# Kernel tuning notes

Measured on AMD Instinct MI355X. Metric: run time of the kernel, lower is better.

## Reference

```python
import jax, jax.numpy as jnp
import numpy as np
from jax import lax

HIDDEN = 10
LAYERS = 5
IN_SIZE = 2
OUT_SIZE = 1
BATCH = 4096
SEQ = 512


def _lstm_layer(xs, h0, c0, W_ih, W_hh, b):
    # xs: [T, B, in], h0/c0: [B, H], W_ih: [4H, in], W_hh: [4H, H], b: [4H]
    def step(carry, x_t):
        h, c = carry
        g = x_t @ W_ih.T + h @ W_hh.T + b  # [B, 4H]
        i, f, gg, o = jnp.split(g, 4, axis=-1)  # torch gate order: i, f, g, o
        i = jax.nn.sigmoid(i)
        f = jax.nn.sigmoid(f)
        gg = jnp.tanh(gg)
        o = jax.nn.sigmoid(o)
        c_new = f * c + i * gg
        h_new = o * jnp.tanh(c_new)
        return (h_new, c_new), h_new

    (hT, cT), hs = lax.scan(step, (h0, c0), xs)
    return hs, hT, cT


def setup_inputs() -> dict:
    key = jax.random.key(0)
    ks = jax.random.split(key, 8)
    s = 1.0 / np.sqrt(HIDDEN)  # torch LSTM init scale
    x = jax.random.normal(ks[0], (BATCH, SEQ, IN_SIZE), dtype=jnp.float32)
    h = jnp.zeros((LAYERS, BATCH, HIDDEN), dtype=jnp.float32)
    c = jnp.zeros((LAYERS, BATCH, HIDDEN), dtype=jnp.float32)
    W_ih0 = jax.random.uniform(ks[1], (4 * HIDDEN, IN_SIZE), minval=-s, maxval=s, dtype=jnp.float32)
    W_ih_rest = jax.random.uniform(ks[2], (LAYERS - 1, 4 * HIDDEN, HIDDEN), minval=-s, maxval=s, dtype=jnp.float32)
    W_hh = jax.random.uniform(ks[3], (LAYERS, 4 * HIDDEN, HIDDEN), minval=-s, maxval=s, dtype=jnp.float32)
    # combined b_ih + b_hh (mathematically identical to torch's two biases)
    b = jax.random.uniform(ks[4], (LAYERS, 4 * HIDDEN), minval=-2 * s, maxval=2 * s, dtype=jnp.float32)
    Wf = jax.random.uniform(ks[5], (OUT_SIZE, HIDDEN), minval=-s, maxval=s, dtype=jnp.float32)
    bf = jax.random.uniform(ks[6], (OUT_SIZE,), minval=-s, maxval=s, dtype=jnp.float32)
    return {"x": x, "h": h, "c": c, "W_ih0": W_ih0, "W_ih_rest": W_ih_rest,
            "W_hh": W_hh, "b": b, "Wf": Wf, "bf": bf}


def reference(x, h, c, W_ih0, W_ih_rest, W_hh, b, Wf, bf):
    xs = jnp.transpose(x, (1, 0, 2))  # [T, B, in] (batch_first -> time-major)
    h_outs, c_outs = [], []
    hs, hT, cT = _lstm_layer(xs, h[0], c[0], W_ih0, W_hh[0], b[0])
    h_outs.append(hT); c_outs.append(cT)
    for l in range(1, LAYERS):
        hs, hT, cT = _lstm_layer(hs, h[l], c[l], W_ih_rest[l - 1], W_hh[l], b[l])
        h_outs.append(hT); c_outs.append(cT)
    L1 = jnp.transpose(hs, (1, 0, 2))  # [B, T, H]
    out = jax.nn.sigmoid(L1 @ Wf.T + bf)  # [B, T, 1]
    return out, (jnp.stack(h_outs), jnp.stack(c_outs))
```

## Files before the change

### kernel.cpp

```cpp
#include <hip/hip_runtime.h>

#define B_ 4096
#define T_ 512
#define H_ 10
#define L_ 5
#define LOG2E 1.44269504f

#define SLOTF(g)   ((g) * 12)
#define TRASH_OFF  72
#define XBUF_OFF   88
#define XENT       520
#define LDS_FLOATS (XBUF_OFF + XENT * 4)

__device__ __forceinline__ float sigm2(float xs) {
    return __builtin_amdgcn_rcpf(1.0f + __builtin_amdgcn_exp2f(-xs));
}
__device__ __forceinline__ float tanh2(float xs) {
    return fmaf(-2.0f, __builtin_amdgcn_rcpf(__builtin_amdgcn_exp2f(xs) + 1.0f), 1.0f);
}

#define DOT10(acc, W, A, Bv, Cv)                              \
    acc = fmaf(W[0], A.x,  acc); acc = fmaf(W[1], A.y,  acc); \
    acc = fmaf(W[2], A.z,  acc); acc = fmaf(W[3], A.w,  acc); \
    acc = fmaf(W[4], Bv.x, acc); acc = fmaf(W[5], Bv.y, acc); \
    acc = fmaf(W[6], Bv.z, acc); acc = fmaf(W[7], Bv.w, acc); \
    acc = fmaf(W[8], Cv.x, acc); acc = fmaf(W[9], Cv.y, acc);

#define GATES(S, GUARD, OUTST)                                                 \
  {                                                                            \
    const float4 xA = *(const float4*)(prevp);                                 \
    const float4 xB = *(const float4*)(prevp + 4);                             \
    const float2 xC = *(const float2*)(prevp + 8);                             \
    const float4 hA = *(const float4*)(ownp);                                  \
    const float4 hB = *(const float4*)(ownp + 4);                              \
    const float2 hC = *(const float2*)(ownp + 8);                              \
    float a0 = bs4[0], a1 = bs4[1], a2 = bs4[2], a3 = bs4[3];                  \
    DOT10(a0, wih[0], xA, xB, xC)                                              \
    DOT10(a1, wih[1], xA, xB, xC)                                              \
    DOT10(a2, wih[2], xA, xB, xC)                                              \
    DOT10(a3, wih[3], xA, xB, xC)                                              \
    DOT10(a0, whh[0], hA, hB, hC)                                              \
    DOT10(a1, whh[1], hA, hB, hC)                                              \
    DOT10(a2, whh[2], hA, hB, hC)                                              \
    DOT10(a3, whh[3], hA, hB, hC)                                              \
    const float ig = sigm2(a0), fg = sigm2(a1);                                \
    const float gg = tanh2(a2), og = sigm2(a3);                                \
    const float cn = fmaf(fg, c, ig * gg);                                     \
    const float hn = og * tanh2(cn * (2.0f * LOG2E));                          \
    if (GUARD) {                                                               \
      const int tl = (S) - g;                                                  \
      const bool valid = (unsigned)tl < (unsigned)T_;                          \
      float* wrt = valid ? wrp : trashp;                                       \
      *wrt = hn;                                                               \
      if (valid) c = cn;                                                       \
      if ((g < 5) && (tl == T_ - 1)) {                                         \
        out[(size_t)(B_ * T_) + g * (B_ * H_) + b * H_ + j] = hn;              \
        out[(size_t)(B_ * T_) + (size_t)(L_ * B_ * H_)                         \
            + g * (B_ * H_) + b * H_ + j] = cn;                                \
      }                                                                        \
    } else {                                                                   \
      *wrp = hn;                                                               \
      c = cn;                                                                  \
    }                                                                          \
    if (OUTST) {                                                               \
      if (g == 5) out[(size_t)b * T_ + ((S) - 5)] = ig;                        \
    }                                                                          \
    prevp += pinc;                                                             \
  }

__global__ __launch_bounds__(64, 3)
void lstm5(const float* __restrict__ x,
           const float* __restrict__ h0,
           const float* __restrict__ c0,
           const float* __restrict__ Wih0,
           const float* __restrict__ WihR,
           const float* __restrict__ Whh,
           const float* __restrict__ bias,
           const float* __restrict__ Wf,
           const float* __restrict__ bfp,
           float* __restrict__ out)
{
    __shared__ __align__(16) float lds[LDS_FLOATS];

    const int lane = threadIdx.x;
    const int g = lane / 10;
    const int j = lane - g * 10;
    const int b = blockIdx.x;

    {
        const float2* x2 = (const float2*)(x + (size_t)b * (T_ * 2));
        #pragma unroll
        for (int i = 0; i < 8; ++i) {
            const int idx = i * 64 + lane;
            float2 v = x2[idx];
            *(float4*)&lds[XBUF_OFF + idx * 4] = make_float4(v.x, v.y, 0.0f, 0.0f);
        }
        if (lane < 8)  lds[XBUF_OFF + 512 * 4 + lane] = 0.0f;
        if (lane < 12) lds[SLOTF(5) + lane] = 0.0f;
    }

    const float scq[4] = {LOG2E, LOG2E, 2.0f * LOG2E, LOG2E};
    float wih[4][10], whh[4][10], bs4[4];
    #pragma unroll
    for (int q = 0; q < 4; ++q) {
        bs4[q] = 0.0f;
        #pragma unroll
        for (int k = 0; k < 10; ++k) { wih[q][k] = 0.0f; whh[q][k] = 0.0f; }
    }
    if (g < 5) {
        #pragma unroll
        for (int q = 0; q < 4; ++q) {
            const int row = q * H_ + j;
            const float sc = scq[q];
            bs4[q] = bias[g * 40 + row] * sc;
            #pragma unroll
            for (int k = 0; k < 10; ++k)
                whh[q][k] = Whh[g * 400 + row * 10 + k] * sc;
            if (g == 0) {
                wih[q][0] = Wih0[row * 2 + 0] * sc;
                wih[q][1] = Wih0[row * 2 + 1] * sc;
            } else {
                #pragma unroll
                for (int k = 0; k < 10; ++k)
                    wih[q][k] = WihR[(g - 1) * 400 + row * 10 + k] * sc;
            }
        }
    } else if (g == 5) {
        #pragma unroll
        for (int k = 0; k < 10; ++k) wih[0][k] = Wf[k] * LOG2E;
        bs4[0] = bfp[0] * LOG2E;
    }

    float c = 0.0f;
    if (g < 5) {
        c = c0[g * (B_ * H_) + b * H_ + j];
        lds[SLOTF(g) + j] = h0[g * (B_ * H_) + b * H_ + j];
    }
    __syncthreads();

    float* ownp  = &lds[(g < 5) ? SLOTF(g) : SLOTF(5)];
    float* prevp = (g == 0) ? &lds[XBUF_OFF]
                 : (g <= 5) ? &lds[SLOTF(g - 1)]
                            : &lds[SLOTF(5)];
    float* wrp   = (g < 5) ? &lds[SLOTF(g) + j]
                           : &lds[TRASH_OFF + (lane - 50)];
    float* trashp = &lds[TRASH_OFF + (lane & 15)];
    const int pinc = (g == 0) ? 4 : 0;

    for (int s = 0; s < 5; ++s)        GATES(s, true,  false)
    for (int s = 5; s <= 510; ++s)     GATES(s, false, true )
    for (int s = 511; s <= 516; ++s)   GATES(s, true,  true )
}

extern "C" void kernel_launch(void* const* d_in, const int* in_sizes, int n_in,
                              void* d_out, int out_size, void* d_ws, size_t ws_size,
                              hipStream_t stream) {
    const float* x    = (const float*)d_in[0];
    const float* h0   = (const float*)d_in[1];
    const float* c0   = (const float*)d_in[2];
    const float* Wih0 = (const float*)d_in[3];
    const float* WihR = (const float*)d_in[4];
    const float* Whh  = (const float*)d_in[5];
    const float* bias = (const float*)d_in[6];
    const float* Wf   = (const float*)d_in[7];
    const float* bf   = (const float*)d_in[8];
    float* out = (float*)d_out;

    dim3 grid(B_);
    dim3 block(64);
    hipLaunchKernelGGL(lstm5, grid, block, 0, stream,
                       x, h0, c0, Wih0, WihR, Whh, bias, Wf, bf, out);
}
```

Measured before the change: 375.1 us.

## Process two batch rows per wavefront using packed FP32 FMA instructions

```diff
diff --git a/kernel.cpp b/kernel.cpp
--- a/kernel.cpp
+++ b/kernel.cpp
@@ -1,4 +1,7 @@
 #include <hip/hip_runtime.h>
+
+typedef float v2f __attribute__((ext_vector_type(2)));
+typedef float v4f __attribute__((ext_vector_type(4)));
 
 #define B_ 4096
 #define T_ 512
@@ -6,69 +9,99 @@
 #define L_ 5
 #define LOG2E 1.44269504f
 
-#define SLOTF(g)   ((g) * 12)
-#define TRASH_OFF  72
-#define XBUF_OFF   88
-#define XENT       520
-#define LDS_FLOATS (XBUF_OFF + XENT * 4)
-
-__device__ __forceinline__ float sigm2(float xs) {
-    return __builtin_amdgcn_rcpf(1.0f + __builtin_amdgcn_exp2f(-xs));
-}
-__device__ __forceinline__ float tanh2(float xs) {
-    return fmaf(-2.0f, __builtin_amdgcn_rcpf(__builtin_amdgcn_exp2f(xs) + 1.0f), 1.0f);
-}
-
-#define DOT10(acc, W, A, Bv, Cv)                              \
-    acc = fmaf(W[0], A.x,  acc); acc = fmaf(W[1], A.y,  acc); \
-    acc = fmaf(W[2], A.z,  acc); acc = fmaf(W[3], A.w,  acc); \
-    acc = fmaf(W[4], Bv.x, acc); acc = fmaf(W[5], Bv.y, acc); \
-    acc = fmaf(W[6], Bv.z, acc); acc = fmaf(W[7], Bv.w, acc); \
-    acc = fmaf(W[8], Cv.x, acc); acc = fmaf(W[9], Cv.y, acc);
-
-#define GATES(S, GUARD, OUTST)                                                 \
-  {                                                                            \
-    const float4 xA = *(const float4*)(prevp);                                 \
-    const float4 xB = *(const float4*)(prevp + 4);                             \
-    const float2 xC = *(const float2*)(prevp + 8);                             \
-    const float4 hA = *(const float4*)(ownp);                                  \
-    const float4 hB = *(const float4*)(ownp + 4);                              \
-    const float2 hC = *(const float2*)(ownp + 8);                              \
-    float a0 = bs4[0], a1 = bs4[1], a2 = bs4[2], a3 = bs4[3];                  \
-    DOT10(a0, wih[0], xA, xB, xC)                                              \
-    DOT10(a1, wih[1], xA, xB, xC)                                              \
-    DOT10(a2, wih[2], xA, xB, xC)                                              \
-    DOT10(a3, wih[3], xA, xB, xC)                                              \
-    DOT10(a0, whh[0], hA, hB, hC)                                              \
-    DOT10(a1, whh[1], hA, hB, hC)                                              \
-    DOT10(a2, whh[2], hA, hB, hC)                                              \
-    DOT10(a3, whh[3], hA, hB, hC)                                              \
-    const float ig = sigm2(a0), fg = sigm2(a1);                                \
-    const float gg = tanh2(a2), og = sigm2(a3);                                \
-    const float cn = fmaf(fg, c, ig * gg);                                     \
-    const float hn = og * tanh2(cn * (2.0f * LOG2E));                          \
-    if (GUARD) {                                                               \
-      const int tl = (S) - g;                                                  \
-      const bool valid = (unsigned)tl < (unsigned)T_;                          \
-      float* wrt = valid ? wrp : trashp;                                       \
-      *wrt = hn;                                                               \
-      if (valid) c = cn;                                                       \
-      if ((g < 5) && (tl == T_ - 1)) {                                         \
-        out[(size_t)(B_ * T_) + g * (B_ * H_) + b * H_ + j] = hn;              \
-        out[(size_t)(B_ * T_) + (size_t)(L_ * B_ * H_)                         \
-            + g * (B_ * H_) + b * H_ + j] = cn;                                \
-      }                                                                        \
-    } else {                                                                   \
-      *wrp = hn;                                                               \
-      c = cn;                                                                  \
-    }                                                                          \
-    if (OUTST) {                                                               \
-      if (g == 5) out[(size_t)b * T_ + ((S) - 5)] = ig;                        \
-    }                                                                          \
-    prevp += pinc;                                                             \
+#define SLOTF(g)   ((g) * 28)
+#define TRASH_F    168
+#define XBUF_F     200
+#define LDS_FLOATS (XBUF_F + 520 * 4)
+
+__device__ __forceinline__ v2f pk_fma(v2f a, v2f b, v2f c) {
+    v2f d;
+    asm("v_pk_fma_f32 %0, %1, %2, %3" : "=v"(d) : "v"(a), "v"(b), "v"(c));
+    return d;
+}
+__device__ __forceinline__ v2f pk_mul(v2f a, v2f b) {
+    v2f d;
+    asm("v_pk_mul_f32 %0, %1, %2" : "=v"(d) : "v"(a), "v"(b));
+    return d;
+}
+__device__ __forceinline__ v2f pk_add(v2f a, v2f b) {
+    v2f d;
+    asm("v_pk_add_f32 %0, %1, %2" : "=v"(d) : "v"(a), "v"(b));
+    return d;
+}
+
+__device__ __forceinline__ v2f sigm2p(v2f xs) {
+    v2f r;
+    r.x = __builtin_amdgcn_rcpf(1.0f + __builtin_amdgcn_exp2f(-xs.x));
+    r.y = __builtin_amdgcn_rcpf(1.0f + __builtin_amdgcn_exp2f(-xs.y));
+    return r;
+}
+__device__ __forceinline__ v2f tanh2p(v2f xs) {
+    v2f r;
+    r.x = fmaf(-2.0f, __builtin_amdgcn_rcpf(__builtin_amdgcn_exp2f(xs.x) + 1.0f), 1.0f);
+    r.y = fmaf(-2.0f, __builtin_amdgcn_rcpf(__builtin_amdgcn_exp2f(xs.y) + 1.0f), 1.0f);
+    return r;
+}
+
+#define DOTX(acc, W)                                                  \
+    acc = pk_fma(W[0], q0.lo, acc); acc = pk_fma(W[1], q0.hi, acc);   \
+    acc = pk_fma(W[2], q1.lo, acc); acc = pk_fma(W[3], q1.hi, acc);   \
+    acc = pk_fma(W[4], q2.lo, acc); acc = pk_fma(W[5], q2.hi, acc);   \
+    acc = pk_fma(W[6], q3.lo, acc); acc = pk_fma(W[7], q3.hi, acc);   \
+    acc = pk_fma(W[8], q4.lo, acc); acc = pk_fma(W[9], q4.hi, acc);
+#define DOTH(acc, W)                                                  \
+    acc = pk_fma(W[0], r0.lo, acc); acc = pk_fma(W[1], r0.hi, acc);   \
+    acc = pk_fma(W[2], r1.lo, acc); acc = pk_fma(W[3], r1.hi, acc);   \
+    acc = pk_fma(W[4], r2.lo, acc); acc = pk_fma(W[5], r2.hi, acc);   \
+    acc = pk_fma(W[6], r3.lo, acc); acc = pk_fma(W[7], r3.hi, acc);   \
+    acc = pk_fma(W[8], r4.lo, acc); acc = pk_fma(W[9], r4.hi, acc);
+
+#define GATES(S, GUARD, OUTST)                                               \
+  {                                                                          \
+    const v4f q0 = *(const v4f*)(prevp);                                     \
+    const v4f q1 = *(const v4f*)(prevp2);                                    \
+    const v4f q2 = *(const v4f*)(prevp2 + 4);                                \
+    const v4f q3 = *(const v4f*)(prevp2 + 8);                                \
+    const v4f q4 = *(const v4f*)(prevp2 + 12);                               \
+    const v4f r0 = *(const v4f*)(ownp);                                      \
+    const v4f r1 = *(const v4f*)(ownp + 4);                                  \
+    const v4f r2 = *(const v4f*)(ownp + 8);                                  \
+    const v4f r3 = *(const v4f*)(ownp + 12);                                 \
+    const v4f r4 = *(const v4f*)(ownp + 16);                                 \
+    v2f a0 = bs2[0], a1 = bs2[1], a2 = bs2[2], a3 = bs2[3];                  \
+    v2f h0a = zero2, h1a = zero2, h2a = zero2, h3a = zero2;                  \
+    DOTX(a0, wih2[0]) DOTX(a1, wih2[1]) DOTX(a2, wih2[2]) DOTX(a3, wih2[3])  \
+    DOTH(h0a, whh2[0]) DOTH(h1a, whh2[1])                                    \
+    DOTH(h2a, whh2[2]) DOTH(h3a, whh2[3])                                    \
+    a0 = pk_add(a0, h0a); a1 = pk_add(a1, h1a);                              \
+    a2 = pk_add(a2, h2a); a3 = pk_add(a3, h3a);                              \
+    const v2f ig = sigm2p(a0), fg = sigm2p(a1);                              \
+    const v2f gg = tanh2p(a2), og = sigm2p(a3);                              \
+    const v2f cn = pk_fma(fg, c, pk_mul(ig, gg));                            \
+    const v2f hn = pk_mul(og, tanh2p(pk_mul(cn, two_l2e)));                  \
+    if (GUARD) {                                                             \
+      const int tl = (S) - g;                                                \
+      const bool valid = (unsigned)tl < (unsigned)T_;                        \
+      float* wrt = valid ? wrp : trashp;                                     \
+      *(v2f*)wrt = hn;                                                       \
+      if (valid) c = cn;                                                     \
+      if ((g < 5) && (tl == T_ - 1)) {                                       \
+        const size_t o1 = (size_t)(B_ * T_) + (size_t)g * (B_ * H_)          \
+                          + (size_t)b2 * H_ + j;                             \
+        out[o1]      = hn.x;  out[o1 + H_]      = hn.y;                      \
+        out[o1 + CO] = cn.x;  out[o1 + CO + H_] = cn.y;                      \
+      }                                                                      \
+    } else {                                                                 \
+      *(v2f*)wrp = hn;                                                       \
+      c = cn;                                                                \
+    }                                                                        \
+    if (OUTST) {                                                             \
+      if (doout) outp[(S) - 5] = (j == 0) ? ig.x : ig.y;                     \
+    }                                                                        \
+    prevp += pinc;                                                           \
   }
 
-__global__ __launch_bounds__(64, 3)
+__global__ __launch_bounds__(64, 2)
 void lstm5(const float* __restrict__ x,
            const float* __restrict__ h0,
            const float* __restrict__ c0,
@@ -85,67 +118,92 @@
     const int lane = threadIdx.x;
     const int g = lane / 10;
     const int j = lane - g * 10;
-    const int b = blockIdx.x;
+    const int b2 = blockIdx.x * 2;
+    const size_t CO = (size_t)L_ * B_ * H_;
+    const v2f zero2 = (v2f)(0.0f);
+    const v2f two_l2e = (v2f){2.0f * LOG2E, 2.0f * LOG2E};
 
     {
-        const float2* x2 = (const float2*)(x + (size_t)b * (T_ * 2));
+        const float2* xA2 = (const float2*)(x + (size_t)b2 * (T_ * 2));
+        const float2* xB2 = (const float2*)(x + (size_t)(b2 + 1) * (T_ * 2));
         #pragma unroll
         for (int i = 0; i < 8; ++i) {
-            const int idx = i * 64 + lane;
-            float2 v = x2[idx];
-            *(float4*)&lds[XBUF_OFF + idx * 4] = make_float4(v.x, v.y, 0.0f, 0.0f);
+            const int t = i * 64 + lane;
+            const float2 a = xA2[t];
+            const float2 bb = xB2[t];
+            *(v4f*)&lds[XBUF_F + t * 4] = (v4f){a.x, bb.x, a.y, bb.y};
         }
-        if (lane < 8)  lds[XBUF_OFF + 512 * 4 + lane] = 0.0f;
-        if (lane < 12) lds[SLOTF(5) + lane] = 0.0f;
+        if (lane < 8) *(v4f*)&lds[XBUF_F + (512 + lane) * 4] = (v4f)(0.0f);
+        if (lane < 32) lds[TRASH_F + lane] = 0.0f;
     }
 
     const float scq[4] = {LOG2E, LOG2E, 2.0f * LOG2E, LOG2E};
-    float wih[4][10], whh[4][10], bs4[4];
+    v2f wih2[4][10], whh2[4][10], bs2[4];
     #pragma unroll
     for (int q = 0; q < 4; ++q) {
-        bs4[q] = 0.0f;
-        #pragma unroll
-        for (int k = 0; k < 10; ++k) { wih[q][k] = 0.0f; whh[q][k] = 0.0f; }
+        bs2[q] = zero2;
+        #pragma unroll
+        for (int k = 0; k < 10; ++k) { wih2[q][k] = zero2; whh2[q][k] = zero2; }
     }
     if (g < 5) {
         #pragma unroll
         for (int q = 0; q < 4; ++q) {
             const int row = q * H_ + j;
             const float sc = scq[q];
-            bs4[q] = bias[g * 40 + row] * sc;
+            const float bv = bias[g * 40 + row] * sc;
+            bs2[q] = (v2f){bv, bv};
             #pragma unroll
-            for (int k = 0; k < 10; ++k)
-                whh[q][k] = Whh[g * 400 + row * 10 + k] * sc;
+            for (int k = 0; k < 10; ++k) {
+                const float w = Whh[g * 400 + row * 10 + k] * sc;
+                whh2[q][k] = (v2f){w, w};
+            }
             if (g == 0) {
-                wih[q][0] = Wih0[row * 2 + 0] * sc;
-                wih[q][1] = Wih0[row * 2 + 1] * sc;
+                const float w0 = Wih0[row * 2 + 0] * sc;
+                const float w1 = Wih0[row * 2 + 1] * sc;
+                wih2[q][0] = (v2f){w0, w0};
+                wih2[q][1] = (v2f){w1, w1};
             } else {
                 #pragma unroll
-                for (int k = 0; k < 10; ++k)
-                    wih[q][k] = WihR[(g - 1) * 400 + row * 10 + k] * sc;
+                for (int k = 0; k < 10; ++k) {
+                    const float w = WihR[(g - 1) * 400 + row * 10 + k] * sc;
+                    wih2[q][k] = (v2f){w, w};
+                }
             }
         }
     } else if (g == 5) {
         #pragma unroll
-        for (int k = 0; k < 10; ++k) wih[0][k] = Wf[k] * LOG2E;
-        bs4[0] = bfp[0] * LOG2E;
-    }
-
-    float c = 0.0f;
+        for (int k = 0; k < 10; ++k) {
+            const float w = Wf[k] * LOG2E;
+            wih2[0][k] = (v2f){w, w};
+        }
+        const float bv = bfp[0] * LOG2E;
+        bs2[0] = (v2f){bv, bv};
+    }
+
+    v2f c = zero2;
     if (g < 5) {
-        c = c0[g * (B_ * H_) + b * H_ + j];
-        lds[SLOTF(g) + j] = h0[g * (B_ * H_) + b * H_ + j];
+        const int base = g * (B_ * H_) + b2 * H_ + j;
+        c.x = c0[base];
+        c.y = c0[base + H_];
+        v2f h00;
+        h00.x = h0[base];
+        h00.y = h0[base + H_];
+        *(v2f*)&lds[SLOTF(g) + 2 * j] = h00;
     }
     __syncthreads();
 
-    float* ownp  = &lds[(g < 5) ? SLOTF(g) : SLOTF(5)];
-    float* prevp = (g == 0) ? &lds[XBUF_OFF]
+    float* const slotbase = (g < 5) ? &lds[SLOTF(g)] : &lds[TRASH_F];
+    float* ownp  = slotbase;
+    float* prevp = (g == 0) ? &lds[XBUF_F]
                  : (g <= 5) ? &lds[SLOTF(g - 1)]
-                            : &lds[SLOTF(5)];
-    float* wrp   = (g < 5) ? &lds[SLOTF(g) + j]
-                           : &lds[TRASH_OFF + (lane - 50)];
-    float* trashp = &lds[TRASH_OFF + (lane & 15)];
+                            : &lds[TRASH_F];
+    float* prevp2 = (g == 0 || g > 5) ? &lds[TRASH_F] : prevp + 4;
+    float* wrp    = slotbase + 2 * j;
+    float* trashp = &lds[TRASH_F] + 2 * (lane & 7);
     const int pinc = (g == 0) ? 4 : 0;
+
+    const bool doout = (g == 5) && (j < 2);
+    float* outp = out + (size_t)(b2 + j) * T_;
 
     for (int s = 0; s < 5; ++s)        GATES(s, true,  false)
     for (int s = 5; s <= 510; ++s)     GATES(s, false, true )
@@ -166,7 +224,7 @@
     const float* bf   = (const float*)d_in[8];
     float* out = (float*)d_out;
 
-    dim3 grid(B_);
+    dim3 grid(B_ / 2);
     dim3 block(64);
     hipLaunchKernelGGL(lstm5, grid, block, 0, stream,
                        x, h0, c0, Wih0, WihR, Whh, bias, Wf, bf, out);
```

Result: faster. 334.3 us (-10.9%).
